# Kernel tuning notes

Measured on AMD Instinct MI355X. Metric: run time of the kernel, lower is better.

Reference implementation:

```python
import jax, jax.numpy as jnp
import numpy as np

MARGIN = 0.2  # init kwarg
_EPS = 1e-12


def _pairwise_dist(x):
    # Euclidean cdist via the Gram trick; safe sqrt so grads stay finite at d=0.
    sq = jnp.sum(x * x, axis=1)
    d2 = sq[:, None] + sq[None, :] - 2.0 * (x @ x.T)
    d2 = jnp.maximum(d2, 0.0)
    safe = jnp.where(d2 > _EPS, d2, _EPS)
    return jnp.where(d2 > _EPS, jnp.sqrt(safe), 0.0)


def setup_inputs() -> dict:
    key = jax.random.key(0)
    k1, k2 = jax.random.split(key)
    B, D = 8192, 128
    embeddings = jax.random.normal(k1, (B, D), dtype=jnp.float32)
    labels = jax.random.randint(k2, (B,), 0, 64)
    return {"embeddings": embeddings, "labels": labels}


def reference(embeddings, labels):
    B = embeddings.shape[0]
    d = _pairwise_dist(embeddings)                      # [B, B]
    eq = labels[None, :] == labels[:, None]             # [B, B] bool (incl. diag)
    pos_mask = eq.astype(d.dtype) - jnp.eye(B, dtype=d.dtype)  # positives, no self
    hardest_positive = jnp.max(d * pos_mask, axis=1)    # [B]
    max_dist = jnp.max(d)
    # push non-negatives (same label, incl. self) out of the min
    hardest_negative = jnp.min(d + max_dist * eq.astype(d.dtype), axis=1)  # [B]
    losses = jax.nn.relu(hardest_positive - hardest_negative + MARGIN)
    return jnp.mean(losses)
```

## Files before the change

### kernel.cpp

```cpp
#include <hip/hip_runtime.h>
#include <hip/hip_bf16.h>


#define BB 8192
#define DD 128
#define MARGIN 0.2f
#define EPS 1e-12f

#define COLS_PER_BLOCK 512
#define ROWS_PER_BLOCK 128
#define STAGE_COLS 32
#define NSTAGES 16
#define STAGE_SHORTS (STAGE_COLS * DD)

typedef __attribute__((ext_vector_type(8))) short short8;
typedef __attribute__((ext_vector_type(4))) float f32x4;

__device__ inline unsigned short f2bf(float f) {
    __hip_bfloat16 h = __float2bfloat16(f);
    unsigned short u;
    __builtin_memcpy(&u, &h, 2);
    return u;
}

__global__ __launch_bounds__(256) void prep_kernel(
    const float* __restrict__ x, const int* __restrict__ lab,
    unsigned short* __restrict__ xb, float2* __restrict__ meta,
    unsigned* __restrict__ hp2, unsigned* __restrict__ mn2,
    unsigned long long* __restrict__ fsum, unsigned* __restrict__ fdone) {
    int t = blockIdx.x * blockDim.x + threadIdx.x;
    int row = t >> 5;
    const float4 v = reinterpret_cast<const float4*>(x)[t];

    union { unsigned short u[4]; uint2 w; } p;
    p.u[0] = f2bf(v.x); p.u[1] = f2bf(v.y);
    p.u[2] = f2bf(v.z); p.u[3] = f2bf(v.w);
    reinterpret_cast<uint2*>(xb)[t] = p.w;

    float s = v.x * v.x + v.y * v.y + v.z * v.z + v.w * v.w;
    #pragma unroll
    for (int m = 16; m >= 1; m >>= 1) s += __shfl_xor(s, m, 64);
    if ((t & 31) == 0) meta[row] = make_float2(s, __int_as_float(lab[row]));

    if (t < BB) { hp2[t] = 0u; mn2[t] = 0x7f800000u; }
    if (t == 0) { *fsum = 0ull; *fdone = 0u; }
}

__global__ __launch_bounds__(512) void triplet_main(
    const unsigned short* __restrict__ xb, const float2* __restrict__ meta,
    unsigned* __restrict__ hp2, unsigned* __restrict__ mn2) {
    const int tid  = threadIdx.x;
    const int wave = tid >> 6;
    const int lane = tid & 63;
    const int l15  = lane & 15;
    const int lhi  = lane >> 4;
    const int rbase = blockIdx.x * ROWS_PER_BLOCK + wave * 16;
    const int cbase = blockIdx.y * COLS_PER_BLOCK;

    __shared__ unsigned short sb[3][STAGE_SHORTS];
    __shared__ float2 smeta[COLS_PER_BLOCK];

    short8 a[4];
    {
        const unsigned short* ar = xb + (size_t)(rbase + l15) * DD + lhi * 8;
        #pragma unroll
        for (int s = 0; s < 4; ++s)
            a[s] = *reinterpret_cast<const short8*>(ar + s * 32);
    }

    unsigned liw = 0;
    {
        #pragma unroll
        for (int k = 0; k < 4; ++k)
            liw |= ((unsigned)__float_as_int(meta[rbase + lhi * 4 + k].y) & 255u) << (8 * k);
    }
    float hp[4], mn[4];
    #pragma unroll
    for (int r = 0; r < 4; ++r) { hp[r] = -__builtin_inff(); mn[r] = __builtin_inff(); }

    smeta[tid] = meta[cbase + tid];

    auto stage = [&](int g, int buf) {
        const char* src_base = (const char*)(xb + (size_t)(cbase + g * STAGE_COLS) * DD);
        const int o   = tid * 16;
        const int row = o >> 8;
        const int byt = (o & 255) ^ ((row & 15) << 4);
        const char* src = src_base + row * 256 + byt;
        char* dst = (char*)&sb[buf][0] + wave * 1024;
        __builtin_amdgcn_global_load_lds(
            (const __attribute__((address_space(1))) void*)src,
            (__attribute__((address_space(3))) void*)dst, 16, 0, 0);
    };

    auto compute_group = [&](int st, int gg, const char* base) {
        const int jl = gg * 16 + l15;
        const int rowoff = jl * 256;
        const int swz = (jl & 15) << 4;
        short8 b[4];
        #pragma unroll
        for (int s = 0; s < 4; ++s)
            b[s] = *reinterpret_cast<const short8*>(
                base + rowoff + ((s * 64 + lhi * 16) ^ swz));
        f32x4 acc = {};
        #pragma unroll
        for (int s = 0; s < 4; ++s)
            acc = __builtin_amdgcn_mfma_f32_16x16x32_bf16(a[s], b[s], acc, 0, 0, 0);

        const float2 mj = smeta[st * STAGE_COLS + jl];
        const float sqj = mj.x;
        const int   lj  = __float_as_int(mj.y) & 255;
        #pragma unroll
        for (int r = 0; r < 4; ++r) {
            const float d2p = fmaf(acc[r], -2.0f, sqj);
            const bool eq = (int)((liw >> (8 * r)) & 255u) == lj;
            hp[r] = fmaxf(hp[r], eq ? d2p : -__builtin_inff());
            mn[r] = fminf(mn[r], eq ? __builtin_inff() : d2p);
        }
    };

    stage(0, 0);
    stage(1, 1);
    #pragma unroll
    for (int st = 0; st < NSTAGES; ++st) {
        if (st < NSTAGES - 1)
            asm volatile("s_waitcnt lgkmcnt(0) vmcnt(1)" ::: "memory");
        else
            asm volatile("s_waitcnt lgkmcnt(0) vmcnt(0)" ::: "memory");
        __builtin_amdgcn_s_barrier();
        __builtin_amdgcn_sched_barrier(0);
        if (st + 2 < NSTAGES) stage(st + 2, (st + 2) % 3);
        const char* base = (const char*)&sb[st % 3][0];
        compute_group(st, 0, base);
        __builtin_amdgcn_sched_barrier(0);
        compute_group(st, 1, base);
    }

    #pragma unroll
    for (int r = 0; r < 4; ++r) {
        const float sqi = meta[rbase + lhi * 4 + r].x;
        hp[r] = fmaxf(sqi + hp[r], 0.0f);
        mn[r] = sqi + mn[r];
    }
    #pragma unroll
    for (int m = 1; m < 16; m <<= 1) {
        #pragma unroll
        for (int r = 0; r < 4; ++r) {
            hp[r] = fmaxf(hp[r], __shfl_xor(hp[r], m, 64));
            mn[r] = fminf(mn[r], __shfl_xor(mn[r], m, 64));
        }
    }
    if (l15 == 0) {
        #pragma unroll
        for (int r = 0; r < 4; ++r) {
            const int i = rbase + lhi * 4 + r;
            atomicMax(&hp2[i], __float_as_uint(hp[r]));
            atomicMin(&mn2[i], __float_as_uint(mn[r]));
        }
    }
}

__device__ inline float d_of(float d2) {
    return (d2 > EPS) ? sqrtf(d2) : 0.0f;
}

__global__ __launch_bounds__(1024) void finalize_kernel(
    const unsigned* __restrict__ hp2, const unsigned* __restrict__ mn2,
    unsigned long long* __restrict__ fsum, unsigned* __restrict__ fdone,
    float* __restrict__ out) {
    const int i = blockIdx.x * 1024 + threadIdx.x;
    const float hpv = d_of(__uint_as_float(hp2[i]));
    const float mnv = d_of(__uint_as_float(mn2[i]));
    float acc = fmaxf(hpv - mnv + MARGIN, 0.0f);

    #pragma unroll
    for (int m = 1; m < 64; m <<= 1) acc += __shfl_xor(acc, m, 64);
    __shared__ float ws[16];
    const int wave = threadIdx.x >> 6;
    if ((threadIdx.x & 63) == 0) ws[wave] = acc;
    __syncthreads();
    if (threadIdx.x == 0) {
        float s = 0.0f;
        #pragma unroll
        for (int w = 0; w < 16; ++w) s += ws[w];
        atomicAdd(fsum, (unsigned long long)((double)s * 4294967296.0));
        __threadfence();
        const unsigned old = atomicAdd(fdone, 1u);
        if (old == gridDim.x - 1) {
            const unsigned long long total = atomicAdd(fsum, 0ull);
            out[0] = (float)((double)total / 4294967296.0 / (double)BB);
        }
    }
}

extern "C" void kernel_launch(void* const* d_in, const int* in_sizes, int n_in,
                              void* d_out, int out_size, void* d_ws, size_t ws_size,
                              hipStream_t stream) {
    const float* x = (const float*)d_in[0];
    const int* lab = (const int*)d_in[1];
    float* out = (float*)d_out;

    char* ws = (char*)d_ws;
    unsigned short* xb = (unsigned short*)ws;
    float2* meta = (float2*)(ws + (size_t)BB * DD * 2);
    unsigned* hp2 = (unsigned*)(ws + (size_t)BB * DD * 2 + BB * 8);
    unsigned* mn2 = (unsigned*)(ws + (size_t)BB * DD * 2 + BB * 12);
    unsigned long long* fsum = (unsigned long long*)(ws + (size_t)BB * DD * 2 + BB * 16);
    unsigned* fdone = (unsigned*)(ws + (size_t)BB * DD * 2 + BB * 16 + 8);

    prep_kernel<<<(BB * DD / 4) / 256, 256, 0, stream>>>(x, lab, xb, meta, hp2, mn2, fsum, fdone);
    dim3 grid(BB / ROWS_PER_BLOCK, BB / COLS_PER_BLOCK);
    triplet_main<<<grid, 512, 0, stream>>>(xb, meta, hp2, mn2);
    finalize_kernel<<<BB / 1024, 1024, 0, stream>>>(hp2, mn2, fsum, fdone, out);
}
```

Measured before the change: 40.16 us.

## Exploit distance symmetry by computing only upper-triangular tiles with column-side reductions

Replaces the full B×B tile grid with a triangular grid of 128×128 tiles. Each tile updates both the row-side hardest positive/negative and, by symmetry, the column-side values through per-column shuffles and global atomics. This roughly halves the MFMA and global-to-LDS load work. In exchange it adds many more per-column atomics, extra ALU and shuffle work per group, a short loop to map the block index to a tile pair, and much smaller blocks (only 4 stages each), which leaves less room to hide pipeline startup.

```diff
diff --git a/kernel.cpp b/kernel.cpp
--- a/kernel.cpp
+++ b/kernel.cpp
@@ -7,10 +7,11 @@
 #define MARGIN 0.2f
 #define EPS 1e-12f
 
-#define COLS_PER_BLOCK 512
-#define ROWS_PER_BLOCK 128
+#define TILE 128
+#define NBLKT (BB / TILE)
+#define NTRI (NBLKT * (NBLKT + 1) / 2)
 #define STAGE_COLS 32
-#define NSTAGES 16
+#define NSTAGES (TILE / STAGE_COLS)
 #define STAGE_SHORTS (STAGE_COLS * DD)
 
 typedef __attribute__((ext_vector_type(8))) short short8;
@@ -54,11 +55,15 @@
     const int lane = tid & 63;
     const int l15  = lane & 15;
     const int lhi  = lane >> 4;
-    const int rbase = blockIdx.x * ROWS_PER_BLOCK + wave * 16;
-    const int cbase = blockIdx.y * COLS_PER_BLOCK;
+
+    int bi = 0, rem = (int)blockIdx.x;
+    while (rem >= NBLKT - bi) { rem -= NBLKT - bi; ++bi; }
+    const int bj = bi + rem;
+    const int rbase = bi * TILE + wave * 16;
+    const int cbase = bj * TILE;
 
     __shared__ unsigned short sb[3][STAGE_SHORTS];
-    __shared__ float2 smeta[COLS_PER_BLOCK];
+    __shared__ float2 smeta[TILE];
 
     short8 a[4];
     {
@@ -69,16 +74,20 @@
     }
 
     unsigned liw = 0;
+    float sqi[4];
     {
         #pragma unroll
-        for (int k = 0; k < 4; ++k)
-            liw |= ((unsigned)__float_as_int(meta[rbase + lhi * 4 + k].y) & 255u) << (8 * k);
+        for (int k = 0; k < 4; ++k) {
+            const float2 mt = meta[rbase + lhi * 4 + k];
+            sqi[k] = mt.x;
+            liw |= ((unsigned)__float_as_int(mt.y) & 255u) << (8 * k);
+        }
     }
     float hp[4], mn[4];
     #pragma unroll
     for (int r = 0; r < 4; ++r) { hp[r] = -__builtin_inff(); mn[r] = __builtin_inff(); }
 
-    smeta[tid] = meta[cbase + tid];
+    if (tid < TILE) smeta[tid] = meta[cbase + tid];
 
     auto stage = [&](int g, int buf) {
         const char* src_base = (const char*)(xb + (size_t)(cbase + g * STAGE_COLS) * DD);
@@ -109,15 +118,29 @@
         const float2 mj = smeta[st * STAGE_COLS + jl];
         const float sqj = mj.x;
         const int   lj  = __float_as_int(mj.y) & 255;
+        float hpc = -__builtin_inff(), mnc = __builtin_inff();
         #pragma unroll
         for (int r = 0; r < 4; ++r) {
             const float d2p = fmaf(acc[r], -2.0f, sqj);
+            const float d2c = fmaf(acc[r], -2.0f, sqi[r]);
             const bool eq = (int)((liw >> (8 * r)) & 255u) == lj;
             hp[r] = fmaxf(hp[r], eq ? d2p : -__builtin_inff());
             mn[r] = fminf(mn[r], eq ? __builtin_inff() : d2p);
+            hpc   = fmaxf(hpc,   eq ? d2c : -__builtin_inff());
+            mnc   = fminf(mnc,   eq ? __builtin_inff() : d2c);
+        }
+        hpc = fmaxf(hpc, __shfl_xor(hpc, 16, 64));
+        hpc = fmaxf(hpc, __shfl_xor(hpc, 32, 64));
+        mnc = fminf(mnc, __shfl_xor(mnc, 16, 64));
+        mnc = fminf(mnc, __shfl_xor(mnc, 32, 64));
+        if (lane < 16) {
+            const int j = cbase + st * STAGE_COLS + jl;
+            atomicMax(&hp2[j], __float_as_uint(fmaxf(sqj + hpc, 0.0f)));
+            atomicMin(&mn2[j], __float_as_uint(sqj + mnc));
         }
     };
 
+    asm volatile("s_waitcnt vmcnt(0)" ::: "memory");
     stage(0, 0);
     stage(1, 1);
     #pragma unroll
@@ -137,9 +160,8 @@
 
     #pragma unroll
     for (int r = 0; r < 4; ++r) {
-        const float sqi = meta[rbase + lhi * 4 + r].x;
-        hp[r] = fmaxf(sqi + hp[r], 0.0f);
-        mn[r] = sqi + mn[r];
+        hp[r] = fmaxf(sqi[r] + hp[r], 0.0f);
+        mn[r] = sqi[r] + mn[r];
     }
     #pragma unroll
     for (int m = 1; m < 16; m <<= 1) {
@@ -208,7 +230,6 @@
     unsigned* fdone = (unsigned*)(ws + (size_t)BB * DD * 2 + BB * 16 + 8);
 
     prep_kernel<<<(BB * DD / 4) / 256, 256, 0, stream>>>(x, lab, xb, meta, hp2, mn2, fsum, fdone);
-    dim3 grid(BB / ROWS_PER_BLOCK, BB / COLS_PER_BLOCK);
-    triplet_main<<<grid, 512, 0, stream>>>(xb, meta, hp2, mn2);
+    triplet_main<<<NTRI, 512, 0, stream>>>(xb, meta, hp2, mn2);
     finalize_kernel<<<BB / 1024, 1024, 0, stream>>>(hp2, mn2, fsum, fdone, out);
 }
```

After: 65.21 us. +62.4%, slower.

## Give each wave private column stream and two row tiles, drop block barriers

Applied to the files above, without the earlier changes.

Each wave now holds A fragments for 32 rows (two 16-row tiles) and reuses every loaded B tile for two MFMA chains. Each wave streams its own 512 columns through a private double-buffered LDS slot, so the block-wide s_barrier per stage is gone. The column metadata is also loaded straight into LDS. The intent is more MFMA work per LDS read and no cross-wave synchronisation. In exchange, different waves in a block no longer share B loads, so global/L2 traffic per block rises, and register pressure increases.

```diff
diff --git a/kernel.cpp b/kernel.cpp
--- a/kernel.cpp
+++ b/kernel.cpp
@@ -7,11 +7,9 @@
 #define MARGIN 0.2f
 #define EPS 1e-12f
 
-#define COLS_PER_BLOCK 512
-#define ROWS_PER_BLOCK 128
-#define STAGE_COLS 32
-#define NSTAGES 16
-#define STAGE_SHORTS (STAGE_COLS * DD)
+#define GCOLS 16
+#define COLS_PER_WAVE 512
+#define NGROUPS (COLS_PER_WAVE / GCOLS)
 
 typedef __attribute__((ext_vector_type(8))) short short8;
 typedef __attribute__((ext_vector_type(4))) float f32x4;
@@ -46,7 +44,7 @@
     if (t == 0) { *fsum = 0ull; *fdone = 0u; }
 }
 
-__global__ __launch_bounds__(512) void triplet_main(
+__global__ __launch_bounds__(256) void triplet_main(
     const unsigned short* __restrict__ xb, const float2* __restrict__ meta,
     unsigned* __restrict__ hp2, unsigned* __restrict__ mn2) {
     const int tid  = threadIdx.x;
@@ -54,107 +52,131 @@
     const int lane = tid & 63;
     const int l15  = lane & 15;
     const int lhi  = lane >> 4;
-    const int rbase = blockIdx.x * ROWS_PER_BLOCK + wave * 16;
-    const int cbase = blockIdx.y * COLS_PER_BLOCK;
-
-    __shared__ unsigned short sb[3][STAGE_SHORTS];
-    __shared__ float2 smeta[COLS_PER_BLOCK];
-
-    short8 a[4];
+
+    const int cc    = blockIdx.x & 15;
+    const int rw    = (blockIdx.x >> 4) * 4 + wave;
+    const int rbase = rw * 32;
+    const int cbase = cc * COLS_PER_WAVE;
+
+    __shared__ unsigned short sbuf[4][2][GCOLS * DD];
+    __shared__ float2 smeta[COLS_PER_WAVE];
+
+    short8 a0[4], a1[4];
     {
-        const unsigned short* ar = xb + (size_t)(rbase + l15) * DD + lhi * 8;
-        #pragma unroll
-        for (int s = 0; s < 4; ++s)
-            a[s] = *reinterpret_cast<const short8*>(ar + s * 32);
-    }
-
-    unsigned liw = 0;
-    {
-        #pragma unroll
-        for (int k = 0; k < 4; ++k)
-            liw |= ((unsigned)__float_as_int(meta[rbase + lhi * 4 + k].y) & 255u) << (8 * k);
-    }
-    float hp[4], mn[4];
-    #pragma unroll
-    for (int r = 0; r < 4; ++r) { hp[r] = -__builtin_inff(); mn[r] = __builtin_inff(); }
-
-    smeta[tid] = meta[cbase + tid];
-
-    auto stage = [&](int g, int buf) {
-        const char* src_base = (const char*)(xb + (size_t)(cbase + g * STAGE_COLS) * DD);
-        const int o   = tid * 16;
-        const int row = o >> 8;
-        const int byt = (o & 255) ^ ((row & 15) << 4);
-        const char* src = src_base + row * 256 + byt;
-        char* dst = (char*)&sb[buf][0] + wave * 1024;
-        __builtin_amdgcn_global_load_lds(
-            (const __attribute__((address_space(1))) void*)src,
-            (__attribute__((address_space(3))) void*)dst, 16, 0, 0);
+        const unsigned short* ar0 = xb + (size_t)(rbase + l15) * DD + lhi * 8;
+        const unsigned short* ar1 = ar0 + 16 * DD;
+        #pragma unroll
+        for (int s = 0; s < 4; ++s) {
+            a0[s] = *reinterpret_cast<const short8*>(ar0 + s * 32);
+            a1[s] = *reinterpret_cast<const short8*>(ar1 + s * 32);
+        }
+    }
+    unsigned li0 = 0, li1 = 0;
+    #pragma unroll
+    for (int k = 0; k < 4; ++k) {
+        li0 |= ((unsigned)__float_as_int(meta[rbase + lhi * 4 + k].y) & 255u) << (8 * k);
+        li1 |= ((unsigned)__float_as_int(meta[rbase + 16 + lhi * 4 + k].y) & 255u) << (8 * k);
+    }
+    float hp0[4], mn0[4], hp1[4], mn1[4];
+    #pragma unroll
+    for (int k = 0; k < 4; ++k) {
+        hp0[k] = -__builtin_inff(); mn0[k] = __builtin_inff();
+        hp1[k] = -__builtin_inff(); mn1[k] = __builtin_inff();
+    }
+
+    auto stage = [&](int g) {
+        const char* sb_ = (const char*)(xb + (size_t)(cbase + g * GCOLS) * DD);
+        char* db = (char*)&sbuf[wave][g & 1][0];
+        #pragma unroll
+        for (int p = 0; p < 4; ++p) {
+            const int o     = p * 1024 + lane * 16;
+            const int col   = o >> 8;
+            const int inner = (o & 255) ^ ((col & 7) << 4);
+            __builtin_amdgcn_global_load_lds(
+                (const __attribute__((address_space(1))) void*)(sb_ + col * 256 + inner),
+                (__attribute__((address_space(3))) void*)(db + p * 1024), 16, 0, 0);
+        }
     };
 
-    auto compute_group = [&](int st, int gg, const char* base) {
-        const int jl = gg * 16 + l15;
-        const int rowoff = jl * 256;
-        const int swz = (jl & 15) << 4;
+    auto body = [&](int g, bool do_stage) {
+        const char* bb_ = (const char*)&sbuf[wave][g & 1][0];
         short8 b[4];
         #pragma unroll
         for (int s = 0; s < 4; ++s)
             b[s] = *reinterpret_cast<const short8*>(
-                base + rowoff + ((s * 64 + lhi * 16) ^ swz));
-        f32x4 acc = {};
-        #pragma unroll
-        for (int s = 0; s < 4; ++s)
-            acc = __builtin_amdgcn_mfma_f32_16x16x32_bf16(a[s], b[s], acc, 0, 0, 0);
-
-        const float2 mj = smeta[st * STAGE_COLS + jl];
-        const float sqj = mj.x;
-        const int   lj  = __float_as_int(mj.y) & 255;
-        #pragma unroll
-        for (int r = 0; r < 4; ++r) {
-            const float d2p = fmaf(acc[r], -2.0f, sqj);
-            const bool eq = (int)((liw >> (8 * r)) & 255u) == lj;
-            hp[r] = fmaxf(hp[r], eq ? d2p : -__builtin_inff());
-            mn[r] = fminf(mn[r], eq ? __builtin_inff() : d2p);
+                bb_ + l15 * 256 + ((s * 64 + lhi * 16) ^ ((l15 & 7) << 4)));
+        const float2 cm = *reinterpret_cast<const float2*>(
+            (const char*)smeta + ((size_t)g * 16 + l15) * 8);
+        asm volatile("s_waitcnt lgkmcnt(0)" ::: "memory");
+        __builtin_amdgcn_sched_barrier(0);
+        if (do_stage) stage(g + 2);
+        f32x4 acc0 = {}, acc1 = {};
+        #pragma unroll
+        for (int s = 0; s < 4; ++s) {
+            acc0 = __builtin_amdgcn_mfma_f32_16x16x32_bf16(a0[s], b[s], acc0, 0, 0, 0);
+            acc1 = __builtin_amdgcn_mfma_f32_16x16x32_bf16(a1[s], b[s], acc1, 0, 0, 0);
+        }
+        const float sqj = cm.x;
+        const int   labj = __float_as_int(cm.y) & 255;
+        #pragma unroll
+        for (int k = 0; k < 4; ++k) {
+            const float d0 = fmaf(acc0[k], -2.0f, sqj);
+            const float d1 = fmaf(acc1[k], -2.0f, sqj);
+            const bool e0 = (int)((li0 >> (8 * k)) & 255u) == labj;
+            const bool e1 = (int)((li1 >> (8 * k)) & 255u) == labj;
+            hp0[k] = fmaxf(hp0[k], e0 ? d0 : -__builtin_inff());
+            mn0[k] = fminf(mn0[k], e0 ? __builtin_inff() : d0);
+            hp1[k] = fmaxf(hp1[k], e1 ? d1 : -__builtin_inff());
+            mn1[k] = fminf(mn1[k], e1 ? __builtin_inff() : d1);
         }
     };
 
-    stage(0, 0);
-    stage(1, 1);
-    #pragma unroll
-    for (int st = 0; st < NSTAGES; ++st) {
-        if (st < NSTAGES - 1)
-            asm volatile("s_waitcnt lgkmcnt(0) vmcnt(1)" ::: "memory");
-        else
-            asm volatile("s_waitcnt lgkmcnt(0) vmcnt(0)" ::: "memory");
-        __builtin_amdgcn_s_barrier();
-        __builtin_amdgcn_sched_barrier(0);
-        if (st + 2 < NSTAGES) stage(st + 2, (st + 2) % 3);
-        const char* base = (const char*)&sb[st % 3][0];
-        compute_group(st, 0, base);
-        __builtin_amdgcn_sched_barrier(0);
-        compute_group(st, 1, base);
-    }
-
-    #pragma unroll
-    for (int r = 0; r < 4; ++r) {
-        const float sqi = meta[rbase + lhi * 4 + r].x;
-        hp[r] = fmaxf(sqi + hp[r], 0.0f);
-        mn[r] = sqi + mn[r];
+    {
+        const char* msrc = (const char*)(meta + cbase);
+        #pragma unroll
+        for (int p = 0; p < 4; ++p)
+            __builtin_amdgcn_global_load_lds(
+                (const __attribute__((address_space(1))) void*)(msrc + p * 1024 + lane * 16),
+                (__attribute__((address_space(3))) void*)((char*)smeta + p * 1024), 16, 0, 0);
+    }
+    stage(0);
+    stage(1);
+
+    for (int g = 0; g < NGROUPS - 2; ++g) {
+        asm volatile("s_waitcnt vmcnt(4)" ::: "memory");
+        body(g, true);
+    }
+    asm volatile("s_waitcnt vmcnt(4)" ::: "memory");
+    body(NGROUPS - 2, false);
+    asm volatile("s_waitcnt vmcnt(0)" ::: "memory");
+    body(NGROUPS - 1, false);
+
+    #pragma unroll
+    for (int k = 0; k < 4; ++k) {
+        const float sqi0 = meta[rbase + lhi * 4 + k].x;
+        const float sqi1 = meta[rbase + 16 + lhi * 4 + k].x;
+        hp0[k] = fmaxf(sqi0 + hp0[k], 0.0f);  mn0[k] = sqi0 + mn0[k];
+        hp1[k] = fmaxf(sqi1 + hp1[k], 0.0f);  mn1[k] = sqi1 + mn1[k];
     }
     #pragma unroll
     for (int m = 1; m < 16; m <<= 1) {
         #pragma unroll
-        for (int r = 0; r < 4; ++r) {
-            hp[r] = fmaxf(hp[r], __shfl_xor(hp[r], m, 64));
-            mn[r] = fminf(mn[r], __shfl_xor(mn[r], m, 64));
+        for (int k = 0; k < 4; ++k) {
+            hp0[k] = fmaxf(hp0[k], __shfl_xor(hp0[k], m, 64));
+            mn0[k] = fminf(mn0[k], __shfl_xor(mn0[k], m, 64));
+            hp1[k] = fmaxf(hp1[k], __shfl_xor(hp1[k], m, 64));
+            mn1[k] = fminf(mn1[k], __shfl_xor(mn1[k], m, 64));
         }
     }
     if (l15 == 0) {
         #pragma unroll
-        for (int r = 0; r < 4; ++r) {
-            const int i = rbase + lhi * 4 + r;
-            atomicMax(&hp2[i], __float_as_uint(hp[r]));
-            atomicMin(&mn2[i], __float_as_uint(mn[r]));
+        for (int k = 0; k < 4; ++k) {
+            const int i0 = rbase + lhi * 4 + k;
+            const int i1 = i0 + 16;
+            atomicMax(&hp2[i0], __float_as_uint(hp0[k]));
+            atomicMin(&mn2[i0], __float_as_uint(mn0[k]));
+            atomicMax(&hp2[i1], __float_as_uint(hp1[k]));
+            atomicMin(&mn2[i1], __float_as_uint(mn1[k]));
         }
     }
 }
@@ -208,7 +230,6 @@
     unsigned* fdone = (unsigned*)(ws + (size_t)BB * DD * 2 + BB * 16 + 8);
 
     prep_kernel<<<(BB * DD / 4) / 256, 256, 0, stream>>>(x, lab, xb, meta, hp2, mn2, fsum, fdone);
-    dim3 grid(BB / ROWS_PER_BLOCK, BB / COLS_PER_BLOCK);
-    triplet_main<<<grid, 512, 0, stream>>>(xb, meta, hp2, mn2);
+    triplet_main<<<1024, 256, 0, stream>>>(xb, meta, hp2, mn2);
     finalize_kernel<<<BB / 1024, 1024, 0, stream>>>(hp2, mn2, fsum, fdone, out);
 }
```

Result: slower. 47.49 us (+18.3%).

## Deepen LDS pipeline, async-load column metadata, remap blocks for XCD locality

Applied to the files above, without the earlier changes.

The column staging buffer grows from 3 to 4 slots, so each block prefetches three stages ahead instead of two, with the vmcnt waits adjusted to match. The per-block column metadata is now loaded asynchronously with global_load_lds instead of a synchronous register round-trip. The 2D grid becomes a 1D grid with a swizzle that maps consecutive blocks on the same XCD to the same column tile, to improve L2 reuse. The cost is more LDS per block, which may lower occupancy, and every wave redundantly loads the same metadata.

```diff
diff --git a/kernel.cpp b/kernel.cpp
--- a/kernel.cpp
+++ b/kernel.cpp
@@ -54,10 +54,15 @@
     const int lane = tid & 63;
     const int l15  = lane & 15;
     const int lhi  = lane >> 4;
-    const int rbase = blockIdx.x * ROWS_PER_BLOCK + wave * 16;
-    const int cbase = blockIdx.y * COLS_PER_BLOCK;
-
-    __shared__ unsigned short sb[3][STAGE_SHORTS];
+
+    const int bid = (int)blockIdx.x;
+    const int swz = (bid & 7) * 128 + (bid >> 3);
+    const int cc  = swz >> 6;
+    const int rb  = swz & 63;
+    const int rbase = rb * ROWS_PER_BLOCK + wave * 16;
+    const int cbase = cc * COLS_PER_BLOCK;
+
+    __shared__ unsigned short sb[4][STAGE_SHORTS];
     __shared__ float2 smeta[COLS_PER_BLOCK];
 
     short8 a[4];
@@ -77,8 +82,6 @@
     float hp[4], mn[4];
     #pragma unroll
     for (int r = 0; r < 4; ++r) { hp[r] = -__builtin_inff(); mn[r] = __builtin_inff(); }
-
-    smeta[tid] = meta[cbase + tid];
 
     auto stage = [&](int g, int buf) {
         const char* src_base = (const char*)(xb + (size_t)(cbase + g * STAGE_COLS) * DD);
@@ -95,12 +98,12 @@
     auto compute_group = [&](int st, int gg, const char* base) {
         const int jl = gg * 16 + l15;
         const int rowoff = jl * 256;
-        const int swz = (jl & 15) << 4;
+        const int swzb = (jl & 15) << 4;
         short8 b[4];
         #pragma unroll
         for (int s = 0; s < 4; ++s)
             b[s] = *reinterpret_cast<const short8*>(
-                base + rowoff + ((s * 64 + lhi * 16) ^ swz));
+                base + rowoff + ((s * 64 + lhi * 16) ^ swzb));
         f32x4 acc = {};
         #pragma unroll
         for (int s = 0; s < 4; ++s)
@@ -108,28 +111,40 @@
 
         const float2 mj = smeta[st * STAGE_COLS + jl];
         const float sqj = mj.x;
-        const int   lj  = __float_as_int(mj.y) & 255;
+        const int   labj = __float_as_int(mj.y) & 255;
         #pragma unroll
         for (int r = 0; r < 4; ++r) {
             const float d2p = fmaf(acc[r], -2.0f, sqj);
-            const bool eq = (int)((liw >> (8 * r)) & 255u) == lj;
+            const bool eq = (int)((liw >> (8 * r)) & 255u) == labj;
             hp[r] = fmaxf(hp[r], eq ? d2p : -__builtin_inff());
             mn[r] = fminf(mn[r], eq ? __builtin_inff() : d2p);
         }
     };
 
+    {
+        const char* msrc = (const char*)(meta + cbase);
+        #pragma unroll
+        for (int p = 0; p < 4; ++p)
+            __builtin_amdgcn_global_load_lds(
+                (const __attribute__((address_space(1))) void*)(msrc + p * 1024 + lane * 16),
+                (__attribute__((address_space(3))) void*)((char*)smeta + p * 1024), 16, 0, 0);
+    }
     stage(0, 0);
     stage(1, 1);
+    stage(2, 2);
+
     #pragma unroll
     for (int st = 0; st < NSTAGES; ++st) {
-        if (st < NSTAGES - 1)
+        if (st < NSTAGES - 2)
+            asm volatile("s_waitcnt lgkmcnt(0) vmcnt(2)" ::: "memory");
+        else if (st == NSTAGES - 2)
             asm volatile("s_waitcnt lgkmcnt(0) vmcnt(1)" ::: "memory");
         else
             asm volatile("s_waitcnt lgkmcnt(0) vmcnt(0)" ::: "memory");
         __builtin_amdgcn_s_barrier();
         __builtin_amdgcn_sched_barrier(0);
-        if (st + 2 < NSTAGES) stage(st + 2, (st + 2) % 3);
-        const char* base = (const char*)&sb[st % 3][0];
+        if (st + 3 < NSTAGES) stage(st + 3, (st + 3) & 3);
+        const char* base = (const char*)&sb[st & 3][0];
         compute_group(st, 0, base);
         __builtin_amdgcn_sched_barrier(0);
         compute_group(st, 1, base);
@@ -208,7 +223,6 @@
     unsigned* fdone = (unsigned*)(ws + (size_t)BB * DD * 2 + BB * 16 + 8);
 
     prep_kernel<<<(BB * DD / 4) / 256, 256, 0, stream>>>(x, lab, xb, meta, hp2, mn2, fsum, fdone);
-    dim3 grid(BB / ROWS_PER_BLOCK, BB / COLS_PER_BLOCK);
-    triplet_main<<<grid, 512, 0, stream>>>(xb, meta, hp2, mn2);
+    triplet_main<<<1024, 512, 0, stream>>>(xb, meta, hp2, mn2);
     finalize_kernel<<<BB / 1024, 1024, 0, stream>>>(hp2, mn2, fsum, fdone, out);
 }
```

Result: no change. 40.68 us (+1.3%).
